# Kernel optimization log

Hardware: AMD Instinct MI355X
Metric: run time of the kernel (lower is better)

The kernel has to match this reference:

```python
import jax, jax.numpy as jnp
import numpy as np

D_MODEL = 1024
N_HEADS = 16
HEAD_DIM = D_MODEL // N_HEADS
BATCH = 1
SEQLEN = 4096


def setup_inputs() -> dict:
    key = jax.random.key(0)
    k1, k2, k3 = jax.random.split(key, 3)
    x = jax.random.normal(k1, (BATCH, SEQLEN, D_MODEL), dtype=jnp.float32)
    # match typical Dense init scale so softmax isn't saturated
    Wqkv = jax.random.normal(k2, (D_MODEL, 3 * D_MODEL), dtype=jnp.float32) / np.sqrt(D_MODEL)
    Wout = jax.random.normal(k3, (D_MODEL, D_MODEL), dtype=jnp.float32) / np.sqrt(D_MODEL)
    return {"x": x, "Wqkv": Wqkv, "Wout": Wout}


def reference(x, Wqkv, Wout):
    b, l, d = x.shape
    qkv = x @ Wqkv  # [b, l, 3d]
    q, k, v = jnp.split(qkv, 3, axis=-1)
    # [b, l, d] -> [b, h, l, hd]
    def to_heads(t):
        return t.reshape(b, l, N_HEADS, HEAD_DIM).transpose(0, 2, 1, 3)
    q, k, v = to_heads(q), to_heads(k), to_heads(v)
    scale = 1.0 / np.sqrt(HEAD_DIM)
    attn = jnp.einsum('bhld,bhsd->bhls', q, k) * scale  # [b,h,l,l]
    causal_mask = jnp.tril(jnp.ones((l, l), dtype=bool))
    attn = jnp.where(causal_mask, attn, -jnp.inf)
    attn = jax.nn.softmax(attn, axis=-1)
    out = jnp.einsum('bhls,bhsd->bhld', attn, v)  # [b,h,l,hd]
    out = out.transpose(0, 2, 1, 3).reshape(b, l, d)
    return out @ Wout
```

## Files before the change

### kernel.cpp

```cpp
#include <hip/hip_runtime.h>

#define SEQ 4096
#define DM 1024
#define NH 16
#define HD 64

typedef __attribute__((ext_vector_type(8))) short short8;
typedef __attribute__((ext_vector_type(4))) short short4v;
typedef __attribute__((ext_vector_type(2))) short short2v;
typedef __attribute__((ext_vector_type(4))) float float4v;
typedef __attribute__((ext_vector_type(4))) int int4v;

__device__ __forceinline__ short f2bf(float f) {
    union { float f; unsigned u; } v; v.f = f;
    unsigned u = v.u;
    return (short)((u + 0x7fffu + ((u >> 16) & 1u)) >> 16);
}
__device__ __forceinline__ int pk2bf(float a, float b) {
    union { float f; unsigned u; } x, y; x.f = a; y.f = b;
    return (int)__builtin_amdgcn_perm(y.u + 0x8000u, x.u + 0x8000u, 0x07060302u);
}

__device__ __forceinline__ void gload_lds16(const void* g, void* l) {
    __builtin_amdgcn_global_load_lds(
        (const __attribute__((address_space(1))) void*)g,
        (__attribute__((address_space(3))) void*)l, 16, 0, 0);
}

__global__ void cast_x(const float* __restrict__ in, short* __restrict__ out, int n4) {
    int i = blockIdx.x * blockDim.x + threadIdx.x;
    if (i < n4) {
        float4v x = ((const float4v*)in)[i];
        short4v o;
        o[0] = f2bf(x[0]); o[1] = f2bf(x[1]); o[2] = f2bf(x[2]); o[3] = f2bf(x[3]);
        ((short4v*)out)[i] = o;
    }
}

__global__ void transpose_cast(const float* __restrict__ in, short* __restrict__ out,
                               int H, int W, int scaled_rows, float scale) {
    __shared__ float tile[32][33];
    int bx = blockIdx.x * 32, by = blockIdx.y * 32;
    int tx = threadIdx.x, ty = threadIdx.y;
#pragma unroll
    for (int i = 0; i < 32; i += 8)
        tile[ty + i][tx] = in[(by + ty + i) * W + bx + tx];
    __syncthreads();
#pragma unroll
    for (int i = 0; i < 32; i += 8) {
        int orow = bx + ty + i;
        float sc = (orow < scaled_rows) ? scale : 1.0f;
        out[orow * H + by + tx] = f2bf(tile[tx][ty + i] * sc);
    }
}

__global__ void transpose_v(const short* __restrict__ qkv, short* __restrict__ vt) {
    __shared__ short tile[64][66];
    int h = blockIdx.z;
    int l0 = blockIdx.x * 64;
    int tx = threadIdx.x, ty = threadIdx.y;
#pragma unroll
    for (int i = 0; i < 8; i++) {
        int r = ty + i * 8;
        short2v v = *(const short2v*)&qkv[(l0 + r) * (3 * DM) + 2 * DM + h * HD + 2 * tx];
        tile[r][2 * tx] = v[0];
        tile[r][2 * tx + 1] = v[1];
    }
    __syncthreads();
#pragma unroll
    for (int i = 0; i < 8; i++) {
        int d = ty + i * 8;
        short2v v;
        v[0] = tile[2 * tx][d];
        v[1] = tile[2 * tx + 1][d];
        int s = l0 + 2 * tx;
        int soff = (s & ~31) | ((s & 12) << 1) | ((s & 16) >> 2) | (s & 3);
        *(short2v*)&vt[(h * HD + d) * SEQ + soff] = v;
    }
}

template <typename OutT>
__global__ __launch_bounds__(256) void gemm_bt(const short* __restrict__ A,
                                               const short* __restrict__ BT,
                                               OutT* __restrict__ C,
                                               int M, int N, int K) {
    __shared__ short As[128 * 32];
    __shared__ short Bs[128 * 32];
    int tid  = threadIdx.x;
    int m0   = blockIdx.y * 128;
    int n0   = blockIdx.x * 128;
    int w    = tid >> 6, lane = tid & 63;
    int wm   = w >> 1,  wn   = w & 1;
    int quad = lane >> 4, l15 = lane & 15;
    int srow = lane >> 2;
    int scol = (lane & 3) * 8;

    float4v acc[4][4];
#pragma unroll
    for (int mi = 0; mi < 4; mi++)
#pragma unroll
        for (int ni = 0; ni < 4; ni++)
            acc[mi][ni] = {0.f, 0.f, 0.f, 0.f};

    for (int k0 = 0; k0 < K; k0 += 32) {
        __syncthreads();
#pragma unroll
        for (int t = 0; t < 2; t++) {
            int chunk = w * 2 + t;
            int r = chunk * 16 + srow;
            gload_lds16(&A[(m0 + r) * K + k0 + scol], &As[chunk * 16 * 32]);
            gload_lds16(&BT[(n0 + r) * K + k0 + scol], &Bs[chunk * 16 * 32]);
        }
        __syncthreads();
        short8 a[4], b[4];
#pragma unroll
        for (int mi = 0; mi < 4; mi++)
            a[mi] = *(const short8*)&As[(wm * 64 + mi * 16 + l15) * 32 + quad * 8];
#pragma unroll
        for (int ni = 0; ni < 4; ni++)
            b[ni] = *(const short8*)&Bs[(wn * 64 + ni * 16 + l15) * 32 + quad * 8];
#pragma unroll
        for (int mi = 0; mi < 4; mi++)
#pragma unroll
            for (int ni = 0; ni < 4; ni++)
                acc[mi][ni] = __builtin_amdgcn_mfma_f32_16x16x32_bf16(a[mi], b[ni], acc[mi][ni], 0, 0, 0);
    }

#pragma unroll
    for (int mi = 0; mi < 4; mi++)
#pragma unroll
        for (int ni = 0; ni < 4; ni++)
#pragma unroll
            for (int r = 0; r < 4; r++) {
                int row = m0 + wm * 64 + mi * 16 + quad * 4 + r;
                int col = n0 + wn * 64 + ni * 16 + l15;
                float v = acc[mi][ni][r];
                if constexpr (sizeof(OutT) == 2) C[row * N + col] = (OutT)f2bf(v);
                else                             C[row * N + col] = (OutT)v;
            }
}

__global__ __launch_bounds__(256) void gemm_bt64(const short* __restrict__ A,
                                                 const short* __restrict__ BT,
                                                 float* __restrict__ C,
                                                 int M, int N, int K) {
    __shared__ short As[64 * 32];
    __shared__ short Bs[128 * 32];
    int tid  = threadIdx.x;
    int m0   = blockIdx.y * 64;
    int n0   = blockIdx.x * 128;
    int w    = tid >> 6, lane = tid & 63;
    int wm   = w >> 1,  wn   = w & 1;
    int quad = lane >> 4, l15 = lane & 15;
    int srow = lane >> 2;
    int scol = (lane & 3) * 8;

    float4v acc[2][4];
#pragma unroll
    for (int mi = 0; mi < 2; mi++)
#pragma unroll
        for (int ni = 0; ni < 4; ni++)
            acc[mi][ni] = {0.f, 0.f, 0.f, 0.f};

    for (int k0 = 0; k0 < K; k0 += 32) {
        __syncthreads();
        {
            int r = w * 16 + srow;
            gload_lds16(&A[(m0 + r) * K + k0 + scol], &As[w * 16 * 32]);
        }
#pragma unroll
        for (int t = 0; t < 2; t++) {
            int chunk = w * 2 + t;
            int r = chunk * 16 + srow;
            gload_lds16(&BT[(n0 + r) * K + k0 + scol], &Bs[chunk * 16 * 32]);
        }
        __syncthreads();
        short8 a[2], b[4];
#pragma unroll
        for (int mi = 0; mi < 2; mi++)
            a[mi] = *(const short8*)&As[(wm * 32 + mi * 16 + l15) * 32 + quad * 8];
#pragma unroll
        for (int ni = 0; ni < 4; ni++)
            b[ni] = *(const short8*)&Bs[(wn * 64 + ni * 16 + l15) * 32 + quad * 8];
#pragma unroll
        for (int mi = 0; mi < 2; mi++)
#pragma unroll
            for (int ni = 0; ni < 4; ni++)
                acc[mi][ni] = __builtin_amdgcn_mfma_f32_16x16x32_bf16(a[mi], b[ni], acc[mi][ni], 0, 0, 0);
    }

#pragma unroll
    for (int mi = 0; mi < 2; mi++)
#pragma unroll
        for (int ni = 0; ni < 4; ni++)
#pragma unroll
            for (int r = 0; r < 4; r++) {
                int row = m0 + wm * 32 + mi * 16 + quad * 4 + r;
                int col = n0 + wn * 64 + ni * 16 + l15;
                C[row * N + col] = acc[mi][ni][r];
            }
}

__global__ __launch_bounds__(256) void attn_kernel(const short* __restrict__ qkv,
                                                   const short* __restrict__ vtp,
                                                   short* __restrict__ aout) {
    __shared__ short Ks[64 * 72];
    __shared__ short Vs[64 * 72];
    int h = blockIdx.x;
    int y = blockIdx.y;
    int t = (y < 16) ? (31 - y) : (y - 16);
    int q0 = t * 128;
    int tid = threadIdx.x;
    int w = tid >> 6, lane = tid & 63;
    int quad = lane >> 4, l15 = lane & 15;
    int qw = q0 + w * 32;
    int r8 = lane >> 3, c8 = lane & 7;
    int srow = w * 16 + r8;

    const short* Kg = qkv + DM + h * HD;
    const short* Vg = vtp + (h * HD) * SEQ;

    short8 aq[2][2];
#pragma unroll
    for (int mi = 0; mi < 2; mi++)
#pragma unroll
        for (int kk = 0; kk < 2; kk++)
            aq[mi][kk] = *(const short8*)&qkv[(qw + mi * 16 + l15) * (3 * DM) + h * HD + kk * 32 + quad * 8];

    float lp[2] = {0.f, 0.f};
    float4v o[2][4];
#pragma unroll
    for (int mi = 0; mi < 2; mi++)
#pragma unroll
        for (int dt = 0; dt < 4; dt++)
            o[mi][dt] = {0.f, 0.f, 0.f, 0.f};

    int nTblk = 2 * t + 2;

    short8 kg[2], vg[2];
#pragma unroll
    for (int i = 0; i < 2; i++) {
        kg[i] = *(const short8*)&Kg[(srow + 8 * i) * (3 * DM) + c8 * 8];
        vg[i] = *(const short8*)&Vg[(srow + 8 * i) * SEQ + c8 * 8];
    }

    for (int tt = 0; tt < nTblk; tt++) {
        int s0 = tt * 64;
        int sn = (tt + 1 < nTblk) ? s0 + 64 : s0;

        __syncthreads();
#pragma unroll
        for (int i = 0; i < 2; i++) {
            *(short8*)&Ks[(srow + 8 * i) * 72 + c8 * 8] = kg[i];
            *(short8*)&Vs[(srow + 8 * i) * 72 + c8 * 8] = vg[i];
        }
#pragma unroll
        for (int i = 0; i < 2; i++) {
            kg[i] = *(const short8*)&Kg[(sn + srow + 8 * i) * (3 * DM) + c8 * 8];
            vg[i] = *(const short8*)&Vg[(srow + 8 * i) * SEQ + sn + c8 * 8];
        }
        __syncthreads();

        short8 kc[8], vc[8];
#pragma unroll
        for (int ni = 0; ni < 4; ni++)
#pragma unroll
            for (int kk = 0; kk < 2; kk++)
                kc[ni * 2 + kk] = *(const short8*)&Ks[(ni * 16 + l15) * 72 + kk * 32 + quad * 8];
#pragma unroll
        for (int dt = 0; dt < 4; dt++)
#pragma unroll
            for (int pr = 0; pr < 2; pr++)
                vc[dt * 2 + pr] = *(const short8*)&Vs[(dt * 16 + l15) * 72 + pr * 32 + quad * 8];

        float4v s[2][4];
#pragma unroll
        for (int mi = 0; mi < 2; mi++)
#pragma unroll
            for (int ni = 0; ni < 4; ni++) {
                float4v a = {0.f, 0.f, 0.f, 0.f};
#pragma unroll
                for (int kk = 0; kk < 2; kk++)
                    a = __builtin_amdgcn_mfma_f32_16x16x32_bf16(kc[ni * 2 + kk], aq[mi][kk], a, 0, 0, 0);
                s[mi][ni] = a;
            }

        bool diag = (s0 + 63 > qw);
        short8 pa[2][2];
#pragma unroll
        for (int mi = 0; mi < 2; mi++) {
            int qrow = qw + mi * 16 + l15;
#pragma unroll
            for (int ni = 0; ni < 4; ni++) {
#pragma unroll
                for (int r = 0; r < 4; r++) {
                    float p = __builtin_amdgcn_exp2f(s[mi][ni][r]);
                    if (diag) {
                        int scol = s0 + ni * 16 + quad * 4 + r;
                        p = (scol <= qrow) ? p : 0.f;
                    }
                    lp[mi] += p;
                    s[mi][ni][r] = p;
                }
            }
#pragma unroll
            for (int pr = 0; pr < 2; pr++) {
                int4v wpk;
                wpk[0] = pk2bf(s[mi][2 * pr][0], s[mi][2 * pr][1]);
                wpk[1] = pk2bf(s[mi][2 * pr][2], s[mi][2 * pr][3]);
                wpk[2] = pk2bf(s[mi][2 * pr + 1][0], s[mi][2 * pr + 1][1]);
                wpk[3] = pk2bf(s[mi][2 * pr + 1][2], s[mi][2 * pr + 1][3]);
                pa[mi][pr] = *(short8*)&wpk;
            }
        }
#pragma unroll
        for (int mi = 0; mi < 2; mi++)
#pragma unroll
            for (int dt = 0; dt < 4; dt++)
#pragma unroll
                for (int pr = 0; pr < 2; pr++)
                    o[mi][dt] = __builtin_amdgcn_mfma_f32_16x16x32_bf16(pa[mi][pr], vc[dt * 2 + pr], o[mi][dt], 0, 0, 0);
    }

#pragma unroll
    for (int mi = 0; mi < 2; mi++) {
        lp[mi] += __shfl_xor(lp[mi], 16, 64);
        lp[mi] += __shfl_xor(lp[mi], 32, 64);
    }
#pragma unroll
    for (int mi = 0; mi < 2; mi++)
#pragma unroll
        for (int r = 0; r < 4; r++) {
            float lr = __shfl(lp[mi], quad * 4 + r, 16);
            float inv = 1.0f / lr;
#pragma unroll
            for (int dt = 0; dt < 4; dt++) {
                float v = o[mi][dt][r] * inv;
                aout[(qw + mi * 16 + quad * 4 + r) * DM + h * HD + dt * 16 + l15] = f2bf(v);
            }
        }
}

extern "C" void kernel_launch(void* const* d_in, const int* in_sizes, int n_in,
                              void* d_out, int out_size, void* d_ws, size_t ws_size,
                              hipStream_t stream) {
    const float* x    = (const float*)d_in[0];
    const float* Wqkv = (const float*)d_in[1];
    const float* Wout = (const float*)d_in[2];
    float* out = (float*)d_out;

    char* ws = (char*)d_ws;
    short* xb    = (short*)(ws);
    short* wqkvT = (short*)(ws + 8388608);
    short* woutT = (short*)(ws + 8388608 + 6291456);
    short* qkv   = (short*)(ws + 16777216);
    short* vt    = (short*)(ws + 16777216 + 25165824);
    short* ao    = (short*)(ws + 16777216 + 25165824 + 8388608);

    const float SC = 0.18033688011112042f;

    cast_x<<<4096, 256, 0, stream>>>(x, xb, (SEQ * DM) / 4);
    transpose_cast<<<dim3(3 * DM / 32, DM / 32), dim3(32, 8), 0, stream>>>(Wqkv, wqkvT, DM, 3 * DM, DM, SC);
    transpose_cast<<<dim3(DM / 32, DM / 32), dim3(32, 8), 0, stream>>>(Wout, woutT, DM, DM, 0, 1.0f);

    gemm_bt<short><<<dim3(3 * DM / 128, SEQ / 128), 256, 0, stream>>>(xb, wqkvT, qkv, SEQ, 3 * DM, DM);

    transpose_v<<<dim3(SEQ / 64, 1, NH), dim3(32, 8), 0, stream>>>(qkv, vt);

    attn_kernel<<<dim3(NH, SEQ / 128), 256, 0, stream>>>(qkv, vt, ao);

    gemm_bt64<<<dim3(DM / 128, SEQ / 64), 256, 0, stream>>>(ao, woutT, out, SEQ, DM, DM);
}
```

Baseline: 216.3 us.

## Split causal attention KV range into two balanced jobs per block with finalize pass

```diff
diff --git a/kernel.cpp b/kernel.cpp
--- a/kernel.cpp
+++ b/kernel.cpp
@@ -203,142 +203,175 @@
 
 __global__ __launch_bounds__(256) void attn_kernel(const short* __restrict__ qkv,
                                                    const short* __restrict__ vtp,
-                                                   short* __restrict__ aout) {
+                                                   float* __restrict__ Of0,
+                                                   float* __restrict__ Of1,
+                                                   float* __restrict__ Lf0,
+                                                   float* __restrict__ Lf1) {
     __shared__ short Ks[64 * 72];
     __shared__ short Vs[64 * 72];
-    int h = blockIdx.x;
-    int y = blockIdx.y;
-    int t = (y < 16) ? (31 - y) : (y - 16);
-    int q0 = t * 128;
+    int gid = blockIdx.x;
+    int rr = gid & 7, qq = gid >> 3;
+    int hb = qq >> 5, b = qq & 31;
+    int h = rr + 8 * hb;
     int tid = threadIdx.x;
     int w = tid >> 6, lane = tid & 63;
     int quad = lane >> 4, l15 = lane & 15;
-    int qw = q0 + w * 32;
     int r8 = lane >> 3, c8 = lane & 7;
     int srow = w * 16 + r8;
 
     const short* Kg = qkv + DM + h * HD;
     const short* Vg = vtp + (h * HD) * SEQ;
 
-    short8 aq[2][2];
-#pragma unroll
-    for (int mi = 0; mi < 2; mi++)
-#pragma unroll
-        for (int kk = 0; kk < 2; kk++)
-            aq[mi][kk] = *(const short8*)&qkv[(qw + mi * 16 + l15) * (3 * DM) + h * HD + kk * 32 + quad * 8];
-
-    float lp[2] = {0.f, 0.f};
-    float4v o[2][4];
-#pragma unroll
-    for (int mi = 0; mi < 2; mi++)
-#pragma unroll
-        for (int dt = 0; dt < 4; dt++)
-            o[mi][dt] = {0.f, 0.f, 0.f, 0.f};
-
-    int nTblk = 2 * t + 2;
-
-    short8 kg[2], vg[2];
-#pragma unroll
-    for (int i = 0; i < 2; i++) {
-        kg[i] = *(const short8*)&Kg[(srow + 8 * i) * (3 * DM) + c8 * 8];
-        vg[i] = *(const short8*)&Vg[(srow + 8 * i) * SEQ + c8 * 8];
-    }
-
-    for (int tt = 0; tt < nTblk; tt++) {
-        int s0 = tt * 64;
-        int sn = (tt + 1 < nTblk) ? s0 + 64 : s0;
-
-        __syncthreads();
+#pragma unroll 1
+    for (int job = 0; job < 2; job++) {
+        int t   = job ? (31 - b) : b;
+        int st0 = job ? (t + 1) : 0;
+        int stN = job ? (2 * t + 2) : (t + 1);
+        float* __restrict__ Of = job ? Of1 : Of0;
+        float* __restrict__ Lf = job ? Lf1 : Lf0;
+        int q0 = t * 128;
+        int qw = q0 + w * 32;
+
+        short8 aq[2][2];
+#pragma unroll
+        for (int mi = 0; mi < 2; mi++)
+#pragma unroll
+            for (int kk = 0; kk < 2; kk++)
+                aq[mi][kk] = *(const short8*)&qkv[(qw + mi * 16 + l15) * (3 * DM) + h * HD + kk * 32 + quad * 8];
+
+        float lp[2] = {0.f, 0.f};
+        float4v o[2][4];
+#pragma unroll
+        for (int mi = 0; mi < 2; mi++)
+#pragma unroll
+            for (int dt = 0; dt < 4; dt++)
+                o[mi][dt] = {0.f, 0.f, 0.f, 0.f};
+
+        short8 kg[2], vg[2];
+        int sb = st0 * 64;
 #pragma unroll
         for (int i = 0; i < 2; i++) {
-            *(short8*)&Ks[(srow + 8 * i) * 72 + c8 * 8] = kg[i];
-            *(short8*)&Vs[(srow + 8 * i) * 72 + c8 * 8] = vg[i];
-        }
-#pragma unroll
-        for (int i = 0; i < 2; i++) {
-            kg[i] = *(const short8*)&Kg[(sn + srow + 8 * i) * (3 * DM) + c8 * 8];
-            vg[i] = *(const short8*)&Vg[(srow + 8 * i) * SEQ + sn + c8 * 8];
-        }
-        __syncthreads();
-
-        short8 kc[8], vc[8];
-#pragma unroll
-        for (int ni = 0; ni < 4; ni++)
-#pragma unroll
-            for (int kk = 0; kk < 2; kk++)
-                kc[ni * 2 + kk] = *(const short8*)&Ks[(ni * 16 + l15) * 72 + kk * 32 + quad * 8];
-#pragma unroll
-        for (int dt = 0; dt < 4; dt++)
-#pragma unroll
-            for (int pr = 0; pr < 2; pr++)
-                vc[dt * 2 + pr] = *(const short8*)&Vs[(dt * 16 + l15) * 72 + pr * 32 + quad * 8];
-
-        float4v s[2][4];
+            kg[i] = *(const short8*)&Kg[(sb + srow + 8 * i) * (3 * DM) + c8 * 8];
+            vg[i] = *(const short8*)&Vg[(srow + 8 * i) * SEQ + sb + c8 * 8];
+        }
+
+        for (int tt = st0; tt < stN; tt++) {
+            int s0 = tt * 64;
+            int sn = (tt + 1 < stN) ? s0 + 64 : s0;
+
+            __syncthreads();
+#pragma unroll
+            for (int i = 0; i < 2; i++) {
+                *(short8*)&Ks[(srow + 8 * i) * 72 + c8 * 8] = kg[i];
+                *(short8*)&Vs[(srow + 8 * i) * 72 + c8 * 8] = vg[i];
+            }
+#pragma unroll
+            for (int i = 0; i < 2; i++) {
+                kg[i] = *(const short8*)&Kg[(sn + srow + 8 * i) * (3 * DM) + c8 * 8];
+                vg[i] = *(const short8*)&Vg[(srow + 8 * i) * SEQ + sn + c8 * 8];
+            }
+            __syncthreads();
+
+            short8 kc[8], vc[8];
+#pragma unroll
+            for (int ni = 0; ni < 4; ni++)
+#pragma unroll
+                for (int kk = 0; kk < 2; kk++)
+                    kc[ni * 2 + kk] = *(const short8*)&Ks[(ni * 16 + l15) * 72 + kk * 32 + quad * 8];
+#pragma unroll
+            for (int dt = 0; dt < 4; dt++)
+#pragma unroll
+                for (int pr = 0; pr < 2; pr++)
+                    vc[dt * 2 + pr] = *(const short8*)&Vs[(dt * 16 + l15) * 72 + pr * 32 + quad * 8];
+
+            float4v s[2][4];
+#pragma unroll
+            for (int mi = 0; mi < 2; mi++)
+#pragma unroll
+                for (int ni = 0; ni < 4; ni++) {
+                    float4v a = {0.f, 0.f, 0.f, 0.f};
+#pragma unroll
+                    for (int kk = 0; kk < 2; kk++)
+                        a = __builtin_amdgcn_mfma_f32_16x16x32_bf16(kc[ni * 2 + kk], aq[mi][kk], a, 0, 0, 0);
+                    s[mi][ni] = a;
+                }
+
+            bool diag = (s0 + 63 > qw);
+            short8 pa[2][2];
+#pragma unroll
+            for (int mi = 0; mi < 2; mi++) {
+                int qrow = qw + mi * 16 + l15;
+#pragma unroll
+                for (int ni = 0; ni < 4; ni++) {
+#pragma unroll
+                    for (int r = 0; r < 4; r++) {
+                        float p = __builtin_amdgcn_exp2f(s[mi][ni][r]);
+                        if (diag) {
+                            int scol = s0 + ni * 16 + quad * 4 + r;
+                            p = (scol <= qrow) ? p : 0.f;
+                        }
+                        lp[mi] += p;
+                        s[mi][ni][r] = p;
+                    }
+                }
+#pragma unroll
+                for (int pr = 0; pr < 2; pr++) {
+                    int4v wpk;
+                    wpk[0] = pk2bf(s[mi][2 * pr][0], s[mi][2 * pr][1]);
+                    wpk[1] = pk2bf(s[mi][2 * pr][2], s[mi][2 * pr][3]);
+                    wpk[2] = pk2bf(s[mi][2 * pr + 1][0], s[mi][2 * pr + 1][1]);
+                    wpk[3] = pk2bf(s[mi][2 * pr + 1][2], s[mi][2 * pr + 1][3]);
+                    pa[mi][pr] = *(short8*)&wpk;
+                }
+            }
+#pragma unroll
+            for (int mi = 0; mi < 2; mi++)
+#pragma unroll
+                for (int dt = 0; dt < 4; dt++)
+#pragma unroll
+                    for (int pr = 0; pr < 2; pr++)
+                        o[mi][dt] = __builtin_amdgcn_mfma_f32_16x16x32_bf16(pa[mi][pr], vc[dt * 2 + pr], o[mi][dt], 0, 0, 0);
+        }
+
+#pragma unroll
+        for (int mi = 0; mi < 2; mi++) {
+            lp[mi] += __shfl_xor(lp[mi], 16, 64);
+            lp[mi] += __shfl_xor(lp[mi], 32, 64);
+        }
 #pragma unroll
         for (int mi = 0; mi < 2; mi++)
 #pragma unroll
-            for (int ni = 0; ni < 4; ni++) {
-                float4v a = {0.f, 0.f, 0.f, 0.f};
-#pragma unroll
-                for (int kk = 0; kk < 2; kk++)
-                    a = __builtin_amdgcn_mfma_f32_16x16x32_bf16(kc[ni * 2 + kk], aq[mi][kk], a, 0, 0, 0);
-                s[mi][ni] = a;
-            }
-
-        bool diag = (s0 + 63 > qw);
-        short8 pa[2][2];
-#pragma unroll
-        for (int mi = 0; mi < 2; mi++) {
-            int qrow = qw + mi * 16 + l15;
-#pragma unroll
-            for (int ni = 0; ni < 4; ni++) {
-#pragma unroll
-                for (int r = 0; r < 4; r++) {
-                    float p = __builtin_amdgcn_exp2f(s[mi][ni][r]);
-                    if (diag) {
-                        int scol = s0 + ni * 16 + quad * 4 + r;
-                        p = (scol <= qrow) ? p : 0.f;
-                    }
-                    lp[mi] += p;
-                    s[mi][ni][r] = p;
-                }
-            }
-#pragma unroll
-            for (int pr = 0; pr < 2; pr++) {
-                int4v wpk;
-                wpk[0] = pk2bf(s[mi][2 * pr][0], s[mi][2 * pr][1]);
-                wpk[1] = pk2bf(s[mi][2 * pr][2], s[mi][2 * pr][3]);
-                wpk[2] = pk2bf(s[mi][2 * pr + 1][0], s[mi][2 * pr + 1][1]);
-                wpk[3] = pk2bf(s[mi][2 * pr + 1][2], s[mi][2 * pr + 1][3]);
-                pa[mi][pr] = *(short8*)&wpk;
-            }
-        }
-#pragma unroll
-        for (int mi = 0; mi < 2; mi++)
-#pragma unroll
-            for (int dt = 0; dt < 4; dt++)
-#pragma unroll
-                for (int pr = 0; pr < 2; pr++)
-                    o[mi][dt] = __builtin_amdgcn_mfma_f32_16x16x32_bf16(pa[mi][pr], vc[dt * 2 + pr], o[mi][dt], 0, 0, 0);
-    }
-
-#pragma unroll
-    for (int mi = 0; mi < 2; mi++) {
-        lp[mi] += __shfl_xor(lp[mi], 16, 64);
-        lp[mi] += __shfl_xor(lp[mi], 32, 64);
-    }
-#pragma unroll
-    for (int mi = 0; mi < 2; mi++)
-#pragma unroll
-        for (int r = 0; r < 4; r++) {
-            float lr = __shfl(lp[mi], quad * 4 + r, 16);
-            float inv = 1.0f / lr;
-#pragma unroll
-            for (int dt = 0; dt < 4; dt++) {
-                float v = o[mi][dt][r] * inv;
-                aout[(qw + mi * 16 + quad * 4 + r) * DM + h * HD + dt * 16 + l15] = f2bf(v);
-            }
-        }
+            for (int r = 0; r < 4; r++) {
+                int row = qw + mi * 16 + quad * 4 + r;
+#pragma unroll
+                for (int dt = 0; dt < 4; dt++)
+                    Of[row * DM + h * HD + dt * 16 + l15] = o[mi][dt][r];
+            }
+        if (quad == 0) {
+#pragma unroll
+            for (int mi = 0; mi < 2; mi++)
+                Lf[h * SEQ + qw + mi * 16 + l15] = lp[mi];
+        }
+    }
+}
+
+__global__ void attn_finalize(const float* __restrict__ Of0, const float* __restrict__ Of1,
+                              const float* __restrict__ Lf0, const float* __restrict__ Lf1,
+                              short* __restrict__ ao) {
+    int i = blockIdx.x * blockDim.x + threadIdx.x;
+    int q  = i >> 8;
+    int c4 = i & 255;
+    int h  = c4 >> 4;
+    float l = Lf0[h * SEQ + q] + Lf1[h * SEQ + q];
+    float inv = 1.0f / l;
+    float4v a = ((const float4v*)Of0)[i];
+    float4v bv = ((const float4v*)Of1)[i];
+    short4v o;
+    o[0] = f2bf((a[0] + bv[0]) * inv);
+    o[1] = f2bf((a[1] + bv[1]) * inv);
+    o[2] = f2bf((a[2] + bv[2]) * inv);
+    o[3] = f2bf((a[3] + bv[3]) * inv);
+    ((short4v*)ao)[i] = o;
 }
 
 extern "C" void kernel_launch(void* const* d_in, const int* in_sizes, int n_in,
@@ -352,10 +385,14 @@
     char* ws = (char*)d_ws;
     short* xb    = (short*)(ws);
     short* wqkvT = (short*)(ws + 8388608);
-    short* woutT = (short*)(ws + 8388608 + 6291456);
+    float* Of0   = (float*)(ws);
     short* qkv   = (short*)(ws + 16777216);
     short* vt    = (short*)(ws + 16777216 + 25165824);
     short* ao    = (short*)(ws + 16777216 + 25165824 + 8388608);
+    float* Of1   = (float*)(ws + 58720256);
+    float* Lf0   = (float*)(ws + 75497472);
+    float* Lf1   = (float*)(ws + 75759616);
+    short* woutT = (short*)(ws + 76021760);
 
     const float SC = 0.18033688011112042f;
 
@@ -367,7 +404,8 @@
 
     transpose_v<<<dim3(SEQ / 64, 1, NH), dim3(32, 8), 0, stream>>>(qkv, vt);
 
-    attn_kernel<<<dim3(NH, SEQ / 128), 256, 0, stream>>>(qkv, vt, ao);
+    attn_kernel<<<512, 256, 0, stream>>>(qkv, vt, Of0, Of1, Lf0, Lf1);
+    attn_finalize<<<(SEQ * DM / 4) / 256, 256, 0, stream>>>(Of0, Of1, Lf0, Lf1, ao);
 
     gemm_bt64<<<dim3(DM / 128, SEQ / 64), 256, 0, stream>>>(ao, woutT, out, SEQ, DM, DM);
 }
```

Result: no change. 214.5 us (-0.8%).
